# Kernel tuning notes

Measured on AMD Instinct MI355X. Metric: run time of the kernel, lower is better.

Reference implementation:

```python
import jax, jax.numpy as jnp
import numpy as np

IN_DIM = 1024
HIDDEN = 1024
NUM_HEAD = 16
HEAD_DIM = HIDDEN // NUM_HEAD
B, S = 4, 2048


def setup_inputs() -> dict:
    key = jax.random.key(0)
    ks = jax.random.split(key, 10)
    sc = 1.0 / np.sqrt(IN_DIM)
    inp = {
        "x": jax.random.normal(ks[0], (B, S, IN_DIM), dtype=jnp.float32),
        "mask": jnp.ones((B, 1, 1, S), dtype=jnp.int32),
        "Wq": jax.random.normal(ks[1], (IN_DIM, HIDDEN), dtype=jnp.float32) * sc,
        "bq": jnp.zeros((HIDDEN,), dtype=jnp.float32),
        "Wk": jax.random.normal(ks[2], (IN_DIM, HIDDEN), dtype=jnp.float32) * sc,
        "bk": jnp.zeros((HIDDEN,), dtype=jnp.float32),
        "Wv": jax.random.normal(ks[3], (IN_DIM, HIDDEN), dtype=jnp.float32) * sc,
        "bv": jnp.zeros((HIDDEN,), dtype=jnp.float32),
        "Wo": jax.random.normal(ks[4], (HIDDEN, IN_DIM), dtype=jnp.float32) * sc,
        "bo": jnp.zeros((IN_DIM,), dtype=jnp.float32),
    }
    return inp


def reference(x, mask, Wq, bq, Wk, bk, Wv, bv, Wo, bo):
    Bq, Sq, _ = x.shape
    # projections -> [B, H, S, hd]
    def proj(W, b):
        return (x @ W + b).reshape(Bq, Sq, NUM_HEAD, HEAD_DIM).transpose(0, 2, 1, 3)
    q, k, v = proj(Wq, bq), proj(Wk, bk), proj(Wv, bv)
    scale = 1.0 / jnp.sqrt(jnp.asarray(HEAD_DIM, dtype=x.dtype))
    scores = jnp.einsum("bhqd,bhkd->bhqk", q, k) * scale  # [B,H,S,S]
    scores = jnp.where(mask == 0, jnp.asarray(-1e9, dtype=x.dtype), scores)
    attn = jax.nn.softmax(scores, axis=-1)
    out = jnp.einsum("bhqk,bhkd->bhqd", attn, v)  # [B,H,S,hd]
    out = out.transpose(0, 2, 1, 3).reshape(Bq, Sq, HIDDEN)
    return out @ Wo + bo
```

## Files before the change

kernel.cpp:

```cpp
#include <hip/hip_runtime.h>
#include <hip/hip_bf16.h>
#include <stdint.h>

#define BB_ 4
#define SS_ 2048
#define IND_ 1024
#define HIDD_ 1024
#define NH_ 16
#define HD_ 64

typedef __attribute__((ext_vector_type(8))) short vshort8;
typedef __attribute__((ext_vector_type(4))) short vshort4;
typedef __attribute__((ext_vector_type(4))) float vfloat4;

__device__ __forceinline__ short bf16_of(float f) {
    union { float f; uint32_t u; } v; v.f = f;
    uint32_t r = v.u + 0x7fffu + ((v.u >> 16) & 1u);
    return (short)(r >> 16);
}

__device__ __forceinline__ uint32_t pk_bf16(float lo, float hi) {
    uint32_t r;
    asm("v_cvt_pk_bf16_f32 %0, %1, %2" : "=v"(r) : "v"(lo), "v"(hi));
    return r;
}

typedef const __attribute__((address_space(1))) uint8_t* gas_ptr;
typedef __attribute__((address_space(3))) uint8_t* las_ptr;
__device__ __forceinline__ void gload16(const void* g, void* l) {
    __builtin_amdgcn_global_load_lds((gas_ptr)g, (las_ptr)l, 16, 0, 0);
}

__global__ __launch_bounds__(256) void conv_x(const float* __restrict__ x,
                                              short* __restrict__ xb, int n4) {
    int i = blockIdx.x * 256 + threadIdx.x;
    if (i >= n4) return;
    float4 v = ((const float4*)x)[i];
    vshort4 r;
    r[0] = bf16_of(v.x); r[1] = bf16_of(v.y); r[2] = bf16_of(v.z); r[3] = bf16_of(v.w);
    ((vshort4*)xb)[i] = r;
}

__global__ __launch_bounds__(256) void convT_w4(const float* __restrict__ W0,
                                                const float* __restrict__ W1,
                                                const float* __restrict__ W2,
                                                const float* __restrict__ W3,
                                                short* __restrict__ T0,
                                                short* __restrict__ T1,
                                                short* __restrict__ T2,
                                                short* __restrict__ T3) {
    const float* W = (blockIdx.z == 0) ? W0 : (blockIdx.z == 1) ? W1 : (blockIdx.z == 2) ? W2 : W3;
    short* Wt = (blockIdx.z == 0) ? T0 : (blockIdx.z == 1) ? T1 : (blockIdx.z == 2) ? T2 : T3;
    __shared__ short tile[64][65];
    int k0 = blockIdx.x * 64, n0 = blockIdx.y * 64;
#pragma unroll
    for (int i = 0; i < 16; i++) {
        int idx = i * 256 + threadIdx.x;
        int r = idx >> 6, c = idx & 63;
        tile[c][r] = bf16_of(W[(k0 + r) * 1024 + n0 + c]);
    }
    __syncthreads();
#pragma unroll
    for (int i = 0; i < 16; i++) {
        int idx = i * 256 + threadIdx.x;
        int r = idx >> 6, c = idx & 63;
        Wt[(n0 + r) * 1024 + k0 + c] = tile[r][c];
    }
}

template <int MODE>
__device__ __forceinline__ void gemm_body(const short* __restrict__ A,
                                          const short* __restrict__ Bt,
                                          const float* __restrict__ bias,
                                          void* __restrict__ out, float scale,
                                          short* smem) {
    constexpr int Kd = 1024;
    const int t = threadIdx.x;
    const int w = t >> 6, lane = t & 63;
    const int g = lane >> 4, c = lane & 15;
    const int wm = w >> 1, wn = w & 1;
    const int m0 = blockIdx.x * 128, n0 = blockIdx.y * 128;

    const int row = t >> 2;
    const int colE = (t & 3) * 8;

    const short* ga0 = A + (size_t)(m0 + row) * Kd + colE;
    const short* ga1 = A + (size_t)(m0 + 64 + row) * Kd + colE;
    const short* gb0 = Bt + (size_t)(n0 + row) * Kd + colE;
    const short* gb1 = Bt + (size_t)(n0 + 64 + row) * Kd + colE;

    vfloat4 acc[4][4] = {};

    gload16(ga0, &smem[t * 8]);
    gload16(ga1, &smem[2048 + t * 8]);
    gload16(gb0, &smem[4096 + t * 8]);
    gload16(gb1, &smem[6144 + t * 8]);
    __syncthreads();

    for (int k0 = 0; k0 < Kd; k0 += 32) {
        const int cur = (k0 >> 5) & 1;
        const int nb = (cur ^ 1) * 8192;
        if (k0 + 32 < Kd) {
            gload16(ga0 + k0 + 32, &smem[nb + t * 8]);
            gload16(ga1 + k0 + 32, &smem[nb + 2048 + t * 8]);
            gload16(gb0 + k0 + 32, &smem[nb + 4096 + t * 8]);
            gload16(gb1 + k0 + 32, &smem[nb + 6144 + t * 8]);
        }
        const int cb = cur * 8192;
        vshort8 af[4], bfr[4];
#pragma unroll
        for (int mi = 0; mi < 4; mi++)
            af[mi] = *(const vshort8*)&smem[cb + (wm * 64 + mi * 16 + c) * 32 + g * 8];
#pragma unroll
        for (int ni = 0; ni < 4; ni++)
            bfr[ni] = *(const vshort8*)&smem[cb + 4096 + (wn * 64 + ni * 16 + c) * 32 + g * 8];
#pragma unroll
        for (int mi = 0; mi < 4; mi++)
#pragma unroll
            for (int ni = 0; ni < 4; ni++)
                acc[mi][ni] = __builtin_amdgcn_mfma_f32_16x16x32_bf16(
                    af[mi], bfr[ni], acc[mi][ni], 0, 0, 0);
        __syncthreads();
    }

#pragma unroll
    for (int ni = 0; ni < 4; ni++) {
        const int n = n0 + wn * 64 + ni * 16 + c;
        const float bv = bias[n];
#pragma unroll
        for (int mi = 0; mi < 4; mi++) {
#pragma unroll
            for (int r = 0; r < 4; r++) {
                const int m = m0 + wm * 64 + mi * 16 + g * 4 + r;
                const float v = (acc[mi][ni][r] + bv) * scale;
                if (MODE == 0) {
                    const int b = m >> 11, s = m & 2047, h = n >> 6, d = n & 63;
                    ((short*)out)[(((size_t)(b * 16 + h)) * 2048 + s) * 64 + d] = bf16_of(v);
                } else {
                    ((float*)out)[(size_t)m * 1024 + n] = v;
                }
            }
        }
    }
}

__global__ __launch_bounds__(256) void gemm_qkv(const short* __restrict__ xb,
                                                const short* __restrict__ Wqt,
                                                const short* __restrict__ Wkt,
                                                const short* __restrict__ Wvt,
                                                const float* __restrict__ bq,
                                                const float* __restrict__ bk,
                                                const float* __restrict__ bv,
                                                short* __restrict__ Qb,
                                                short* __restrict__ Kb,
                                                short* __restrict__ Vb) {
    __shared__ alignas(16) short smem[16384];
    const int z = blockIdx.z;
    const short* Bt = (z == 0) ? Wqt : (z == 1) ? Wkt : Wvt;
    const float* bias = (z == 0) ? bq : (z == 1) ? bk : bv;
    short* out = (z == 0) ? Qb : (z == 1) ? Kb : Vb;
    const float scale = (z == 0) ? 0.125f * 1.4426950408889634f : 1.0f;
    gemm_body<0>(xb, Bt, bias, out, scale, smem);
}

__global__ __launch_bounds__(256) void gemm_out(const short* __restrict__ A,
                                                const short* __restrict__ Bt,
                                                const float* __restrict__ bias,
                                                float* __restrict__ out) {
    __shared__ alignas(16) short smem[16384];
    gemm_body<1>(A, Bt, bias, out, 1.0f, smem);
}

__global__ __launch_bounds__(256) void transpose_v(const short* __restrict__ V,
                                                   short* __restrict__ Vt) {
    __shared__ short tile[64][65];
    const int bh = blockIdx.y;
    const int s0 = blockIdx.x * 64;
#pragma unroll
    for (int i = 0; i < 16; i++) {
        int idx = i * 256 + threadIdx.x;
        int r = idx >> 6, c = idx & 63;
        tile[c][r] = V[((size_t)bh * 2048 + s0 + r) * 64 + c];
    }
    __syncthreads();
#pragma unroll
    for (int i = 0; i < 16; i++) {
        int idx = i * 256 + threadIdx.x;
        int r = idx >> 6, c = idx & 63;
        Vt[((size_t)bh * 64 + r) * 2048 + s0 + c] = tile[r][c];
    }
}

__device__ __forceinline__ vshort8 lds_frag(const short* base, int row, int off) {
    const int byte = row * 128 + (off ^ ((row & 7) << 4));
    return *(const vshort8*)((const char*)base + byte);
}
__device__ __forceinline__ uint2 lds_frag8B(const short* base, int row, int eoff) {
    const int byte = row * 128 + ((eoff * 2) ^ ((row & 7) << 4));
    return *(const uint2*)((const char*)base + byte);
}

__global__ __launch_bounds__(256) void attn_kernel(const short* __restrict__ Q,
                                                   const short* __restrict__ K,
                                                   const short* __restrict__ Vt,
                                                   const int* __restrict__ mask,
                                                   short* __restrict__ Oattn) {
    __shared__ alignas(16) short Kl[2][64 * 64];
    __shared__ alignas(16) short Vl[2][64 * 64];
    const int tid = threadIdx.x, w = tid >> 6, lane = tid & 63;
    const int g = lane >> 4, c = lane & 15;
    const int bh = blockIdx.y, bb = bh >> 4, h = bh & 15;
    const int q0 = blockIdx.x * 128 + w * 32;
    const short* Qb = Q + (size_t)bh * 2048 * 64;
    const short* Kb = K + (size_t)bh * 2048 * 64;
    const short* Vb = Vt + (size_t)bh * 64 * 2048;
    const int* mb = mask + bb * 2048;

    const int srow = tid >> 3, se8 = tid & 7;
    const int srow2 = srow + 32;
    const int sw = (se8 * 8) ^ ((srow & 7) << 3);

    vshort8 qa[2][2];
#pragma unroll
    for (int qt = 0; qt < 2; qt++)
#pragma unroll
        for (int kf = 0; kf < 2; kf++)
            qa[qt][kf] = *(const vshort8*)(Qb + (size_t)(q0 + qt * 16 + c) * 64 + kf * 32 + g * 8);

    vfloat4 o[2][4] = {};
    vfloat4 osum[2] = {};
    const vfloat4 ZF = {0.f, 0.f, 0.f, 0.f};
    vshort8 ONESV;
#pragma unroll
    for (int i = 0; i < 8; i++) ONESV[i] = (short)0x3F80;

    gload16(Kb + (size_t)srow * 64 + sw, (char*)Kl[0] + tid * 16);
    gload16(Kb + (size_t)srow2 * 64 + sw, (char*)Kl[0] + 4096 + tid * 16);
    gload16(Vb + (size_t)srow * 2048 + sw, (char*)Vl[0] + tid * 16);
    gload16(Vb + (size_t)srow2 * 2048 + sw, (char*)Vl[0] + 4096 + tid * 16);
    __syncthreads();

    for (int t = 0; t < 32; t++) {
        const int k0 = t * 64;
        const short* Kc = Kl[t & 1];
        const short* Vc = Vl[t & 1];
        if (t + 1 < 32) {
            const int kn = k0 + 64;
            char* kd = (char*)Kl[(t + 1) & 1];
            char* vd = (char*)Vl[(t + 1) & 1];
            gload16(Kb + (size_t)(kn + srow) * 64 + sw, kd + tid * 16);
            gload16(Kb + (size_t)(kn + srow2) * 64 + sw, kd + 4096 + tid * 16);
            gload16(Vb + (size_t)srow * 2048 + kn + sw, vd + tid * 16);
            gload16(Vb + (size_t)srow2 * 2048 + kn + sw, vd + 4096 + tid * 16);
        }

        const int mv = mb[k0 + lane];
        const bool allone = __all(mv != 0);

        vshort8 kb[4][2];
#pragma unroll
        for (int kt = 0; kt < 4; kt++) {
            kb[kt][0] = lds_frag(Kc, kt * 16 + c, g * 16);
            kb[kt][1] = lds_frag(Kc, kt * 16 + c, 64 + g * 16);
        }
        vfloat4 s[2][4];
        __builtin_amdgcn_s_setprio(1);
#pragma unroll
        for (int qt = 0; qt < 2; qt++)
#pragma unroll
            for (int kt = 0; kt < 4; kt++) {
                vfloat4 z = __builtin_amdgcn_mfma_f32_16x16x32_bf16(kb[kt][0], qa[qt][0], ZF, 0, 0, 0);
                s[qt][kt] = __builtin_amdgcn_mfma_f32_16x16x32_bf16(kb[kt][1], qa[qt][1], z, 0, 0, 0);
            }
        __builtin_amdgcn_s_setprio(0);

        if (!allone) {
#pragma unroll
            for (int kt = 0; kt < 4; kt++)
#pragma unroll
                for (int r = 0; r < 4; r++) {
                    if (mb[k0 + kt * 16 + g * 4 + r] == 0) {
                        s[0][kt][r] = -3e8f;
                        s[1][kt][r] = -3e8f;
                    }
                }
        }

#pragma unroll
        for (int qt = 0; qt < 2; qt++)
#pragma unroll
            for (int kt = 0; kt < 4; kt++)
#pragma unroll
                for (int r = 0; r < 4; r++)
                    s[qt][kt][r] = exp2f(s[qt][kt][r]);

        __builtin_amdgcn_s_setprio(1);
#pragma unroll
        for (int u = 0; u < 2; u++) {
            union { uint32_t uu[4]; vshort8 v; } Pf[2];
#pragma unroll
            for (int qt = 0; qt < 2; qt++) {
                Pf[qt].uu[0] = pk_bf16(s[qt][2 * u][0], s[qt][2 * u][1]);
                Pf[qt].uu[1] = pk_bf16(s[qt][2 * u][2], s[qt][2 * u][3]);
                Pf[qt].uu[2] = pk_bf16(s[qt][2 * u + 1][0], s[qt][2 * u + 1][1]);
                Pf[qt].uu[3] = pk_bf16(s[qt][2 * u + 1][2], s[qt][2 * u + 1][3]);
            }
            const int e0 = (2 * u) * 16 + g * 4;
            const int e1 = (2 * u + 1) * 16 + g * 4;
#pragma unroll
            for (int dt = 0; dt < 4; dt++) {
                const uint2 x0 = lds_frag8B(Vc, dt * 16 + c, e0);
                const uint2 x1 = lds_frag8B(Vc, dt * 16 + c, e1);
                union { uint32_t uu[4]; vshort8 v; } Vf;
                Vf.uu[0] = x0.x; Vf.uu[1] = x0.y; Vf.uu[2] = x1.x; Vf.uu[3] = x1.y;
                o[0][dt] = __builtin_amdgcn_mfma_f32_16x16x32_bf16(Pf[0].v, Vf.v, o[0][dt], 0, 0, 0);
                o[1][dt] = __builtin_amdgcn_mfma_f32_16x16x32_bf16(Pf[1].v, Vf.v, o[1][dt], 0, 0, 0);
            }
            osum[0] = __builtin_amdgcn_mfma_f32_16x16x32_bf16(Pf[0].v, ONESV, osum[0], 0, 0, 0);
            osum[1] = __builtin_amdgcn_mfma_f32_16x16x32_bf16(Pf[1].v, ONESV, osum[1], 0, 0, 0);
        }
        __builtin_amdgcn_s_setprio(0);

        __syncthreads();
    }

#pragma unroll
    for (int qt = 0; qt < 2; qt++)
#pragma unroll
        for (int r = 0; r < 4; r++) {
            const float inv = 1.0f / osum[qt][r];
            const int q = q0 + qt * 16 + g * 4 + r;
#pragma unroll
            for (int dt = 0; dt < 4; dt++) {
                const float v = o[qt][dt][r] * inv;
                Oattn[((size_t)bb * 2048 + q) * 1024 + h * 64 + dt * 16 + c] = bf16_of(v);
            }
        }
}

extern "C" void kernel_launch(void* const* d_in, const int* in_sizes, int n_in,
                              void* d_out, int out_size, void* d_ws, size_t ws_size,
                              hipStream_t stream) {
    const float* x   = (const float*)d_in[0];
    const int*  mask = (const int*)d_in[1];
    const float* Wq  = (const float*)d_in[2];
    const float* bq  = (const float*)d_in[3];
    const float* Wk  = (const float*)d_in[4];
    const float* bk  = (const float*)d_in[5];
    const float* Wv  = (const float*)d_in[6];
    const float* bv  = (const float*)d_in[7];
    const float* Wo  = (const float*)d_in[8];
    const float* bo  = (const float*)d_in[9];
    float* out = (float*)d_out;

    short* xb  = (short*)d_ws;
    short* Wqt = xb + 8192 * 1024;
    short* Wkt = Wqt + 1024 * 1024;
    short* Wvt = Wkt + 1024 * 1024;
    short* Wot = Wvt + 1024 * 1024;
    short* Qb  = Wot + 1024 * 1024;
    short* Kb  = Qb + 8192 * 1024;
    short* Vb  = Kb + 8192 * 1024;
    short* Vtb = Vb + 8192 * 1024;
    short* att = Vtb + 8192 * 1024;

    conv_x<<<8192, 256, 0, stream>>>(x, xb, 8192 * 1024 / 4);
    convT_w4<<<dim3(16, 16, 4), 256, 0, stream>>>(Wq, Wk, Wv, Wo, Wqt, Wkt, Wvt, Wot);

    gemm_qkv<<<dim3(64, 8, 3), 256, 0, stream>>>(xb, Wqt, Wkt, Wvt, bq, bk, bv, Qb, Kb, Vb);

    transpose_v<<<dim3(32, 64), 256, 0, stream>>>(Vb, Vtb);
    attn_kernel<<<dim3(16, 64), 256, 0, stream>>>(Qb, Kb, Vtb, mask, att);

    gemm_out<<<dim3(64, 8), 256, 0, stream>>>(att, Wot, bo, out);
}
```

Before: 237.7 us.

## Shrink attention blocks to two waves and prefetch K/V through registers

The attention kernel now launches 128-thread blocks covering 64 queries (twice as many blocks). It replaces the double-buffered direct global-to-LDS loads with a single LDS buffer, staged each iteration from registers that were prefetched during the previous tile. The aim is to lower LDS use per block and raise occupancy and parallelism, while register prefetch hides global latency. In exchange each block adds a second barrier per iteration and more register pressure, and K/V is reloaded from global memory by twice as many blocks.

```diff
diff --git a/kernel.cpp b/kernel.cpp
--- a/kernel.cpp
+++ b/kernel.cpp
@@ -199,26 +199,28 @@
     const int byte = row * 128 + ((eoff * 2) ^ ((row & 7) << 4));
     return *(const uint2*)((const char*)base + byte);
 }
-
-__global__ __launch_bounds__(256) void attn_kernel(const short* __restrict__ Q,
+__device__ __forceinline__ void lds_stg(short* base, int row, int e8, vshort8 v) {
+    const int byte = row * 128 + ((e8 * 16) ^ ((row & 7) << 4));
+    *(vshort8*)((char*)base + byte) = v;
+}
+
+__global__ __launch_bounds__(128) void attn_kernel(const short* __restrict__ Q,
                                                    const short* __restrict__ K,
                                                    const short* __restrict__ Vt,
                                                    const int* __restrict__ mask,
                                                    short* __restrict__ Oattn) {
-    __shared__ alignas(16) short Kl[2][64 * 64];
-    __shared__ alignas(16) short Vl[2][64 * 64];
+    __shared__ alignas(16) short Kl[64 * 64];
+    __shared__ alignas(16) short Vl[64 * 64];
     const int tid = threadIdx.x, w = tid >> 6, lane = tid & 63;
     const int g = lane >> 4, c = lane & 15;
     const int bh = blockIdx.y, bb = bh >> 4, h = bh & 15;
-    const int q0 = blockIdx.x * 128 + w * 32;
+    const int q0 = blockIdx.x * 64 + w * 32;
     const short* Qb = Q + (size_t)bh * 2048 * 64;
     const short* Kb = K + (size_t)bh * 2048 * 64;
     const short* Vb = Vt + (size_t)bh * 64 * 2048;
     const int* mb = mask + bb * 2048;
 
     const int srow = tid >> 3, se8 = tid & 7;
-    const int srow2 = srow + 32;
-    const int sw = (se8 * 8) ^ ((srow & 7) << 3);
 
     vshort8 qa[2][2];
 #pragma unroll
@@ -234,34 +236,38 @@
 #pragma unroll
     for (int i = 0; i < 8; i++) ONESV[i] = (short)0x3F80;
 
-    gload16(Kb + (size_t)srow * 64 + sw, (char*)Kl[0] + tid * 16);
-    gload16(Kb + (size_t)srow2 * 64 + sw, (char*)Kl[0] + 4096 + tid * 16);
-    gload16(Vb + (size_t)srow * 2048 + sw, (char*)Vl[0] + tid * 16);
-    gload16(Vb + (size_t)srow2 * 2048 + sw, (char*)Vl[0] + 4096 + tid * 16);
-    __syncthreads();
-
-    for (int t = 0; t < 32; t++) {
-        const int k0 = t * 64;
-        const short* Kc = Kl[t & 1];
-        const short* Vc = Vl[t & 1];
-        if (t + 1 < 32) {
+    vshort8 rk[4], rv[4];
+#pragma unroll
+    for (int j = 0; j < 4; j++) {
+        rk[j] = *(const vshort8*)(Kb + (size_t)(srow + 16 * j) * 64 + se8 * 8);
+        rv[j] = *(const vshort8*)(Vb + (size_t)(srow + 16 * j) * 2048 + se8 * 8);
+    }
+
+    for (int k0 = 0; k0 < 2048; k0 += 64) {
+        __syncthreads();
+#pragma unroll
+        for (int j = 0; j < 4; j++) {
+            lds_stg(Kl, srow + 16 * j, se8, rk[j]);
+            lds_stg(Vl, srow + 16 * j, se8, rv[j]);
+        }
+        __syncthreads();
+        if (k0 + 64 < 2048) {
             const int kn = k0 + 64;
-            char* kd = (char*)Kl[(t + 1) & 1];
-            char* vd = (char*)Vl[(t + 1) & 1];
-            gload16(Kb + (size_t)(kn + srow) * 64 + sw, kd + tid * 16);
-            gload16(Kb + (size_t)(kn + srow2) * 64 + sw, kd + 4096 + tid * 16);
-            gload16(Vb + (size_t)srow * 2048 + kn + sw, vd + tid * 16);
-            gload16(Vb + (size_t)srow2 * 2048 + kn + sw, vd + 4096 + tid * 16);
-        }
-
-        const int mv = mb[k0 + lane];
-        const bool allone = __all(mv != 0);
+#pragma unroll
+            for (int j = 0; j < 4; j++) {
+                rk[j] = *(const vshort8*)(Kb + (size_t)(kn + srow + 16 * j) * 64 + se8 * 8);
+                rv[j] = *(const vshort8*)(Vb + (size_t)(srow + 16 * j) * 2048 + kn + se8 * 8);
+            }
+        }
+
+        const int mv = mb[k0 + (lane & 31)];
+        const bool allone = __all(mv != 0) && __all(mb[k0 + 32 + (lane & 31)] != 0);
 
         vshort8 kb[4][2];
 #pragma unroll
         for (int kt = 0; kt < 4; kt++) {
-            kb[kt][0] = lds_frag(Kc, kt * 16 + c, g * 16);
-            kb[kt][1] = lds_frag(Kc, kt * 16 + c, 64 + g * 16);
+            kb[kt][0] = lds_frag(Kl, kt * 16 + c, g * 16);
+            kb[kt][1] = lds_frag(Kl, kt * 16 + c, 64 + g * 16);
         }
         vfloat4 s[2][4];
         __builtin_amdgcn_s_setprio(1);
@@ -309,8 +315,8 @@
             const int e1 = (2 * u + 1) * 16 + g * 4;
 #pragma unroll
             for (int dt = 0; dt < 4; dt++) {
-                const uint2 x0 = lds_frag8B(Vc, dt * 16 + c, e0);
-                const uint2 x1 = lds_frag8B(Vc, dt * 16 + c, e1);
+                const uint2 x0 = lds_frag8B(Vl, dt * 16 + c, e0);
+                const uint2 x1 = lds_frag8B(Vl, dt * 16 + c, e1);
                 union { uint32_t uu[4]; vshort8 v; } Vf;
                 Vf.uu[0] = x0.x; Vf.uu[1] = x0.y; Vf.uu[2] = x1.x; Vf.uu[3] = x1.y;
                 o[0][dt] = __builtin_amdgcn_mfma_f32_16x16x32_bf16(Pf[0].v, Vf.v, o[0][dt], 0, 0, 0);
@@ -320,8 +326,6 @@
             osum[1] = __builtin_amdgcn_mfma_f32_16x16x32_bf16(Pf[1].v, ONESV, osum[1], 0, 0, 0);
         }
         __builtin_amdgcn_s_setprio(0);
-
-        __syncthreads();
     }
 
 #pragma unroll
@@ -370,7 +374,7 @@
     gemm_qkv<<<dim3(64, 8, 3), 256, 0, stream>>>(xb, Wqt, Wkt, Wvt, bq, bk, bv, Qb, Kb, Vb);
 
     transpose_v<<<dim3(32, 64), 256, 0, stream>>>(Vb, Vtb);
-    attn_kernel<<<dim3(16, 64), 256, 0, stream>>>(Qb, Kb, Vtb, mask, att);
+    attn_kernel<<<dim3(32, 64), 128, 0, stream>>>(Qb, Kb, Vtb, mask, att);
 
     gemm_out<<<dim3(64, 8), 256, 0, stream>>>(att, Wot, bo, out);
 }
```

New measurement: 283.9 us. 19.5% more time.
